# Kernel tuning notes

Measured on AMD Instinct MI355X. Metric: run time of the kernel, lower is better.

Reference implementation:

```python
import jax, jax.numpy as jnp
import numpy as np
import math

B, S, D_MODEL, D_K = 4, 4096, 1024, 256

def setup_inputs() -> dict:
    key = jax.random.key(0)
    ks = jax.random.split(key, 9)
    def xavier(k, shape):
        fan_out, fan_in = shape
        limit = math.sqrt(6.0 / (fan_in + fan_out))
        return jax.random.uniform(k, shape, jnp.float32, -limit, limit)
    return {
        "_q": jax.random.normal(ks[0], (B, S, D_MODEL), jnp.float32),
        "_k": jax.random.normal(ks[1], (B, S, D_MODEL), jnp.float32),
        "_v": jax.random.normal(ks[2], (B, S, D_MODEL), jnp.float32),
        "mask": jnp.ones((B, 1, S), dtype=bool),  # unused by the original forward
        "Wq": xavier(ks[3], (D_K, D_MODEL)),
        "bq": jnp.zeros((D_K,), jnp.float32),
        "Wk": xavier(ks[4], (D_K, D_MODEL)),
        "bk": jnp.zeros((D_K,), jnp.float32),
        "Wv": xavier(ks[5], (D_K, D_MODEL)),
        "bv": jnp.zeros((D_K,), jnp.float32),
    }

def reference(_q, _k, _v, mask, Wq, bq, Wk, bk, Wv, bv):
    # Linear projections: x @ W.T + b  (torch nn.Linear semantics)
    q = jnp.einsum('bsm,km->bsk', _q, Wq) + bq  # [B,S,d_k]
    k = jnp.einsum('bsm,km->bsk', _k, Wk) + bk
    v = jnp.einsum('bsm,km->bsk', _v, Wv) + bv
    scores = jnp.einsum('bqk,bsk->bqs', q, k) / math.sqrt(D_K)  # [B,S,S]
    atten = jax.nn.softmax(scores, axis=-1)
    out = jnp.einsum('bqs,bsk->bqk', atten, v)  # [B,S,d_k]
    return out
```

## Files before the change

### kernel.cpp

```cpp
#include <hip/hip_runtime.h>
#include <stdint.h>

#define DEV static __device__ __forceinline__

typedef __bf16 bf16x8 __attribute__((ext_vector_type(8)));
typedef float f32x4 __attribute__((ext_vector_type(4)));

typedef const __attribute__((address_space(1))) void* as1cp;
typedef __attribute__((address_space(3))) void* as3p;

DEV uint32_t f2bf1(float f) {
  uint32_t u = __builtin_bit_cast(uint32_t, f);
  u += 0x7fffu + ((u >> 16) & 1u);
  return u >> 16;
}
DEV uint32_t f2bf2(float lo, float hi) { return f2bf1(lo) | (f2bf1(hi) << 16); }
DEV float bf2f(uint32_t h) { return __builtin_bit_cast(float, h << 16); }

DEV void gll16(const void* g, void* l) {
  __builtin_amdgcn_global_load_lds((as1cp)g, (as3p)l, 16, 0, 0);
}

__global__ __launch_bounds__(256, 3) void proj_kernel(
    const float* __restrict__ xq, const float* __restrict__ xk, const float* __restrict__ xv,
    const float* __restrict__ wq, const float* __restrict__ wk, const float* __restrict__ wv,
    const float* __restrict__ bq, const float* __restrict__ bk, const float* __restrict__ bv,
    uint16_t* __restrict__ qo, uint16_t* __restrict__ ko, uint16_t* __restrict__ vo)
{
  const int z = blockIdx.z;
  const float* X  = (z == 0) ? xq : (z == 1) ? xk : xv;
  const float* W  = (z == 0) ? wq : (z == 1) ? wk : wv;
  const float* Bi = (z == 0) ? bq : (z == 1) ? bk : bv;

  const int tid = threadIdx.x;
  const int lane = tid & 63;
  const int w = tid >> 6;
  const int wm = w >> 1, wn = w & 1;
  const int l15 = lane & 15, g = lane >> 4;
  const int m0 = blockIdx.x * 128;
  const int n0 = blockIdx.y * 128;

  __shared__ uint16_t sA[128 * 64];
  __shared__ uint16_t sB[128 * 64];

  const int am = tid >> 1, ak = (tid & 1) * 32;
  const float* Ap = X + (size_t)(m0 + am) * 1024 + ak;
  const float* Wp = W + (size_t)(n0 + am) * 1024 + ak;

  f32x4 acc[4][4];
  #pragma unroll
  for (int i = 0; i < 4; ++i)
    #pragma unroll
    for (int j = 0; j < 4; ++j) { f32x4 zz = {0.f, 0.f, 0.f, 0.f}; acc[i][j] = zz; }

  float ar[32];
  #pragma unroll
  for (int i = 0; i < 8; ++i) { float4 t = ((const float4*)Ap)[i];
    ar[4*i+0]=t.x; ar[4*i+1]=t.y; ar[4*i+2]=t.z; ar[4*i+3]=t.w; }

  const uint32_t ph = (uint32_t)(am * 128 + ak * 2) ^ ((uint32_t)(am & 7) << 4);

  for (int kt = 0; kt < 16; ++kt) {
    if (kt) __syncthreads();
    #pragma unroll
    for (int c = 0; c < 4; ++c) {
      uint4 p;
      p.x = f2bf2(ar[8*c+0], ar[8*c+1]); p.y = f2bf2(ar[8*c+2], ar[8*c+3]);
      p.z = f2bf2(ar[8*c+4], ar[8*c+5]); p.w = f2bf2(ar[8*c+6], ar[8*c+7]);
      *(uint4*)((char*)sA + (ph ^ (16u * c))) = p;
    }
    {
      float wr[32];
      const float* Wk = Wp + kt * 64;
      #pragma unroll
      for (int i = 0; i < 8; ++i) { float4 t = ((const float4*)Wk)[i];
        wr[4*i+0]=t.x; wr[4*i+1]=t.y; wr[4*i+2]=t.z; wr[4*i+3]=t.w; }
      #pragma unroll
      for (int c = 0; c < 4; ++c) {
        uint4 p;
        p.x = f2bf2(wr[8*c+0], wr[8*c+1]); p.y = f2bf2(wr[8*c+2], wr[8*c+3]);
        p.z = f2bf2(wr[8*c+4], wr[8*c+5]); p.w = f2bf2(wr[8*c+6], wr[8*c+7]);
        *(uint4*)((char*)sB + (ph ^ (16u * c))) = p;
      }
    }
    __syncthreads();
    if (kt < 15) {
      const float* Ap2 = Ap + (kt + 1) * 64;
      #pragma unroll
      for (int i = 0; i < 8; ++i) { float4 t = ((const float4*)Ap2)[i];
        ar[4*i+0]=t.x; ar[4*i+1]=t.y; ar[4*i+2]=t.z; ar[4*i+3]=t.w; }
    }
    #pragma unroll
    for (int ks = 0; ks < 2; ++ks) {
      bf16x8 fa[4], fb[4];
      #pragma unroll
      for (int f = 0; f < 4; ++f) {
        uint32_t row = wm * 64 + 16 * f + l15;
        fa[f] = *(const bf16x8*)((char*)sA + row * 128 +
                 (((uint32_t)(ks * 64 + g * 16)) ^ ((row & 7) << 4)));
      }
      #pragma unroll
      for (int f = 0; f < 4; ++f) {
        uint32_t row = wn * 64 + 16 * f + l15;
        fb[f] = *(const bf16x8*)((char*)sB + row * 128 +
                 (((uint32_t)(ks * 64 + g * 16)) ^ ((row & 7) << 4)));
      }
      #pragma unroll
      for (int fm = 0; fm < 4; ++fm)
        #pragma unroll
        for (int fn = 0; fn < 4; ++fn)
          acc[fm][fn] = __builtin_amdgcn_mfma_f32_16x16x32_bf16(fa[fm], fb[fn], acc[fm][fn], 0, 0, 0);
    }
  }

  #pragma unroll
  for (int fn = 0; fn < 4; ++fn) {
    const int n = n0 + wn * 64 + 16 * fn + l15;
    const float bias = Bi[n];
    #pragma unroll
    for (int fm = 0; fm < 4; ++fm) {
      const int mg = m0 + wm * 64 + 16 * fm + 4 * g;
      if (z == 0) {
        #pragma unroll
        for (int r = 0; r < 4; ++r)
          qo[(size_t)(mg + r) * 256 + n] =
              (uint16_t)f2bf1((acc[fm][fn][r] + bias) * 0.09016844f);
      } else if (z == 1) {
        #pragma unroll
        for (int r = 0; r < 4; ++r)
          ko[(size_t)(mg + r) * 256 + n] = (uint16_t)f2bf1(acc[fm][fn][r] + bias);
      } else {
        uint2 pv;
        pv.x = f2bf2(acc[fm][fn][0] + bias, acc[fm][fn][1] + bias);
        pv.y = f2bf2(acc[fm][fn][2] + bias, acc[fm][fn][3] + bias);
        *(uint2*)(vo + (((size_t)(mg >> 12)) << 20) + (((size_t)n) << 12) + (mg & 4095)) = pv;
      }
    }
  }
}

__global__ __launch_bounds__(512) void attn_kernel(
    const uint16_t* __restrict__ qg, const uint16_t* __restrict__ kg,
    const uint16_t* __restrict__ vg, float* __restrict__ out)
{
  extern __shared__ char smem[];

  const int bid = blockIdx.x;
  const int xcd = bid & 7, slot = bid >> 3;
  const int batch = xcd >> 1;
  const int q0 = (((xcd & 1) << 5) + slot) * 64;

  const int tid = threadIdx.x;
  const int lane = tid & 63;
  const int w = tid >> 6;
  const int hv = w >> 2;
  const int wq = w & 3;
  const int l15 = lane & 15, g = lane >> 4;
  const size_t rowb = (size_t)batch * 4096;

  bf16x8 qf[8];
  {
    const uint16_t* qp = qg + (rowb + q0 + wq * 16 + l15) * 256;
    #pragma unroll
    for (int ks = 0; ks < 8; ++ks) qf[ks] = *(const bf16x8*)(qp + ks * 32 + g * 8);
  }

  f32x4 o[16];
  #pragma unroll
  for (int i = 0; i < 16; ++i) { f32x4 zz = {0.f, 0.f, 0.f, 0.f}; o[i] = zz; }
  float mrow[4], lrow[4];
  #pragma unroll
  for (int r = 0; r < 4; ++r) { mrow[r] = -1e30f; lrow[r] = 0.f; }

  const char* kgb = (const char*)(kg + rowb * 256);
  const char* vgb = (const char*)(vg + (size_t)batch * 256 * 4096);

  auto STAGE = [&](int h, int buf, int t) {
    const int kv0 = (2 * t + h) * 32;
    char* kd = smem + (size_t)(h * 2 + buf) * 16384;
    char* vd = smem + 65536 + (size_t)(h * 2 + buf) * 16384;
    #pragma unroll
    for (int r2 = 0; r2 < 2; ++r2) {
      uint32_t L = (uint32_t)(tid + r2 * 512) * 16;
      uint32_t U = L ^ (((L >> 9) & 7u) << 4);
      gll16(kgb + (size_t)(kv0 + (U >> 9)) * 512 + (U & 511), kd + L);
      uint32_t d = L >> 6;
      uint32_t kvo = (L >> 4) & 3u;
      gll16(vgb + (size_t)d * 8192 + (size_t)(kv0 + 8 * kvo) * 2, vd + L);
    }
  };

  STAGE(0, 0, 0); STAGE(1, 0, 0);
  char* Pw = smem + 131072 + (size_t)w * 1024;
  int buf = 0;

  for (int t = 0; t < 64; ++t) {
    __syncthreads();
    if (t + 1 < 64) { STAGE(0, buf ^ 1, t + 1); STAGE(1, buf ^ 1, t + 1); }

    const char* Kb = smem + (size_t)(hv * 2 + buf) * 16384;
    const char* Vb = smem + 65536 + (size_t)(hv * 2 + buf) * 16384;

    f32x4 s4[2];
    #pragma unroll
    for (int f = 0; f < 2; ++f) { f32x4 zz = {0.f, 0.f, 0.f, 0.f}; s4[f] = zz; }
    #pragma unroll
    for (int ks = 0; ks < 8; ++ks) {
      bf16x8 kf[2];
      #pragma unroll
      for (int f = 0; f < 2; ++f) {
        uint32_t row = 16 * f + l15;
        kf[f] = *(const bf16x8*)(Kb + row * 512 +
                 (((uint32_t)(ks * 64 + g * 16)) ^ ((l15 & 7) << 4)));
      }
      #pragma unroll
      for (int f = 0; f < 2; ++f)
        s4[f] = __builtin_amdgcn_mfma_f32_16x16x32_bf16(qf[ks], kf[f], s4[f], 0, 0, 0);
    }

    float mx[4];
    #pragma unroll
    for (int r = 0; r < 4; ++r) {
      float m2 = fmaxf(s4[0][r], s4[1][r]);
      m2 = fmaxf(m2, __shfl_xor(m2, 1, 64));
      m2 = fmaxf(m2, __shfl_xor(m2, 2, 64));
      m2 = fmaxf(m2, __shfl_xor(m2, 4, 64));
      m2 = fmaxf(m2, __shfl_xor(m2, 8, 64));
      mx[r] = m2;
    }
    int stable = (mx[0] <= mrow[0] + 8.f) && (mx[1] <= mrow[1] + 8.f) &&
                 (mx[2] <= mrow[2] + 8.f) && (mx[3] <= mrow[3] + 8.f);
    if (!__all(stable)) {
      float sc[4];
      #pragma unroll
      for (int r = 0; r < 4; ++r) {
        float mn = fmaxf(mrow[r], mx[r]);
        sc[r] = exp2f(mrow[r] - mn);
        mrow[r] = mn;
        lrow[r] *= sc[r];
      }
      #pragma unroll
      for (int j = 0; j < 16; ++j)
        #pragma unroll
        for (int r = 0; r < 4; ++r) o[j][r] *= sc[r];
    }
    float ps[2][4];
    #pragma unroll
    for (int r = 0; r < 4; ++r) {
      float sum = 0.f;
      #pragma unroll
      for (int f = 0; f < 2; ++f) { ps[f][r] = exp2f(s4[f][r] - mrow[r]); sum += ps[f][r]; }
      sum += __shfl_xor(sum, 1, 64);
      sum += __shfl_xor(sum, 2, 64);
      sum += __shfl_xor(sum, 4, 64);
      sum += __shfl_xor(sum, 8, 64);
      lrow[r] += sum;
    }

    #pragma unroll
    for (int f = 0; f < 2; ++f)
      #pragma unroll
      for (int r = 0; r < 4; ++r)
        *(uint16_t*)(Pw + (4 * g + r) * 64 +
            (((uint32_t)(32 * f + 2 * l15)) ^ ((uint32_t)g << 4))) = (uint16_t)f2bf1(ps[f][r]);

    bf16x8 pa = *(const bf16x8*)(Pw + l15 * 64 + 16 * (g ^ (l15 >> 2)));
    #pragma unroll
    for (int fd = 0; fd < 16; ++fd) {
      bf16x8 vbf = *(const bf16x8*)(Vb + fd * 1024 + l15 * 64 + g * 16);
      o[fd] = __builtin_amdgcn_mfma_f32_16x16x32_bf16(pa, vbf, o[fd], 0, 0, 0);
    }

    buf ^= 1;
  }

  float*    mlb = (float*)smem;
  uint32_t* ob  = (uint32_t*)(smem + 8192);
  __syncthreads();
  if (hv == 1) {
    #pragma unroll
    for (int r = 0; r < 4; ++r) {
      mlb[((0 * 4 + wq) * 64 + lane) * 4 + r] = mrow[r];
      mlb[((1 * 4 + wq) * 64 + lane) * 4 + r] = lrow[r];
    }
    #pragma unroll
    for (int fd = 0; fd < 16; ++fd)
      #pragma unroll
      for (int p = 0; p < 2; ++p)
        ob[(wq * 32 + fd * 2 + p) * 64 + lane] = f2bf2(o[fd][2 * p], o[fd][2 * p + 1]);
  }
  __syncthreads();
  if (hv == 0) {
    float a[4], b2[4], inv[4];
    #pragma unroll
    for (int r = 0; r < 4; ++r) {
      float mu = mlb[((0 * 4 + wq) * 64 + lane) * 4 + r];
      float lu = mlb[((1 * 4 + wq) * 64 + lane) * 4 + r];
      float mn = fmaxf(mrow[r], mu);
      a[r]  = exp2f(mrow[r] - mn);
      b2[r] = exp2f(mu - mn);
      inv[r] = 1.f / (lrow[r] * a[r] + lu * b2[r]);
    }
    float* op = out + (rowb + q0 + wq * 16) * 256;
    #pragma unroll
    for (int fd = 0; fd < 16; ++fd) {
      #pragma unroll
      for (int p = 0; p < 2; ++p) {
        uint32_t u = ob[(wq * 32 + fd * 2 + p) * 64 + lane];
        float vlo = bf2f(u & 0xffffu), vhi = bf2f(u >> 16);
        int r0 = 2 * p, r1 = 2 * p + 1;
        op[(4 * g + r0) * 256 + 16 * fd + l15] =
            (o[fd][r0] * a[r0] + vlo * b2[r0]) * inv[r0];
        op[(4 * g + r1) * 256 + 16 * fd + l15] =
            (o[fd][r1] * a[r1] + vhi * b2[r1]) * inv[r1];
      }
    }
  }
}

extern "C" void kernel_launch(void* const* d_in, const int* in_sizes, int n_in,
                              void* d_out, int out_size, void* d_ws, size_t ws_size,
                              hipStream_t stream) {
  const float* xq = (const float*)d_in[0];
  const float* xk = (const float*)d_in[1];
  const float* xv = (const float*)d_in[2];
  const float* wq = (const float*)d_in[4];
  const float* bq = (const float*)d_in[5];
  const float* wk = (const float*)d_in[6];
  const float* bk = (const float*)d_in[7];
  const float* wv = (const float*)d_in[8];
  const float* bv = (const float*)d_in[9];

  uint16_t* qws = (uint16_t*)d_ws;
  uint16_t* kws = qws + (size_t)4 * 4096 * 256;
  uint16_t* vws = kws + (size_t)4 * 4096 * 256;

  proj_kernel<<<dim3(128, 2, 3), 256, 0, stream>>>(
      xq, xk, xv, wq, wk, wv, bq, bk, bv, qws, kws, vws);

  (void)hipFuncSetAttribute((const void*)attn_kernel,
                            hipFuncAttributeMaxDynamicSharedMemorySize, 139264);
  attn_kernel<<<dim3(256), 512, 139264, stream>>>(qws, kws, vws, (float*)d_out);
}
```

Baseline: 446.6 us.

## Single-buffer attention K/V staging with precomputed offsets and smaller LDS

Replaces the double-buffered K/V LDS pipeline with one buffer that is refilled between two barriers at the end of each iteration. Global source offsets are precomputed once per thread, and V is laid out so each lane reads a contiguous 16-byte chunk. Dynamic shared memory drops from about 139KB to 73KB, and launch bounds now request higher occupancy. The cost is that global-to-LDS loads no longer overlap with MFMA compute; the grid is one block per CU, so the extra occupancy may not be usable. The tighter register budget from the launch bounds may also cause spills.

```diff
diff --git a/kernel.cpp b/kernel.cpp
--- a/kernel.cpp
+++ b/kernel.cpp
@@ -139,7 +139,7 @@
   }
 }
 
-__global__ __launch_bounds__(512) void attn_kernel(
+__global__ __launch_bounds__(512, 4) void attn_kernel(
     const uint16_t* __restrict__ qg, const uint16_t* __restrict__ kg,
     const uint16_t* __restrict__ vg, float* __restrict__ out)
 {
@@ -175,32 +175,34 @@
   const char* kgb = (const char*)(kg + rowb * 256);
   const char* vgb = (const char*)(vg + (size_t)batch * 256 * 4096);
 
-  auto STAGE = [&](int h, int buf, int t) {
-    const int kv0 = (2 * t + h) * 32;
-    char* kd = smem + (size_t)(h * 2 + buf) * 16384;
-    char* vd = smem + 65536 + (size_t)(h * 2 + buf) * 16384;
-    #pragma unroll
-    for (int r2 = 0; r2 < 2; ++r2) {
-      uint32_t L = (uint32_t)(tid + r2 * 512) * 16;
-      uint32_t U = L ^ (((L >> 9) & 7u) << 4);
-      gll16(kgb + (size_t)(kv0 + (U >> 9)) * 512 + (U & 511), kd + L);
-      uint32_t d = L >> 6;
-      uint32_t kvo = (L >> 4) & 3u;
-      gll16(vgb + (size_t)d * 8192 + (size_t)(kv0 + 8 * kvo) * 2, vd + L);
-    }
+  uint32_t ksrc[4], vsrc[4], sdst[4];
+  #pragma unroll
+  for (int r = 0; r < 4; ++r) {
+    uint32_t L = (uint32_t)(r * 512 + tid) * 16;
+    sdst[r] = L;
+    uint32_t row = (L >> 9) & 31, h = L >> 14;
+    ksrc[r] = (32 * h + row) * 512 + ((L & 511) ^ ((row & 7) << 4));
+    uint32_t fd = (L >> 10) & 15, g2 = (L >> 8) & 3, lv = (L >> 4) & 15;
+    vsrc[r] = (fd * 16 + lv) * 8192 + 64 * h + 16 * g2;
+  }
+
+  auto STAGE = [&](int t) {
+    const uint32_t kt = (uint32_t)t * 32768;
+    const uint32_t vt = (uint32_t)t * 128;
+    #pragma unroll
+    for (int r = 0; r < 4; ++r) gll16(kgb + kt + ksrc[r], smem + sdst[r]);
+    #pragma unroll
+    for (int r = 0; r < 4; ++r) gll16(vgb + vt + vsrc[r], smem + 32768 + sdst[r]);
   };
 
-  STAGE(0, 0, 0); STAGE(1, 0, 0);
-  char* Pw = smem + 131072 + (size_t)w * 1024;
-  int buf = 0;
+  STAGE(0);
+  __syncthreads();
+
+  const char* Kb = smem + hv * 16384;
+  const char* Vb = smem + 32768 + hv * 16384;
+  char* Pw = smem + 65536 + (size_t)w * 1024;
 
   for (int t = 0; t < 64; ++t) {
-    __syncthreads();
-    if (t + 1 < 64) { STAGE(0, buf ^ 1, t + 1); STAGE(1, buf ^ 1, t + 1); }
-
-    const char* Kb = smem + (size_t)(hv * 2 + buf) * 16384;
-    const char* Vb = smem + 65536 + (size_t)(hv * 2 + buf) * 16384;
-
     f32x4 s4[2];
     #pragma unroll
     for (int f = 0; f < 2; ++f) { f32x4 zz = {0.f, 0.f, 0.f, 0.f}; s4[f] = zz; }
@@ -267,16 +269,17 @@
     bf16x8 pa = *(const bf16x8*)(Pw + l15 * 64 + 16 * (g ^ (l15 >> 2)));
     #pragma unroll
     for (int fd = 0; fd < 16; ++fd) {
-      bf16x8 vbf = *(const bf16x8*)(Vb + fd * 1024 + l15 * 64 + g * 16);
+      bf16x8 vbf = *(const bf16x8*)(Vb + fd * 1024 + lane * 16);
       o[fd] = __builtin_amdgcn_mfma_f32_16x16x32_bf16(pa, vbf, o[fd], 0, 0, 0);
     }
 
-    buf ^= 1;
+    __syncthreads();
+    if (t + 1 < 64) STAGE(t + 1);
+    __syncthreads();
   }
 
   float*    mlb = (float*)smem;
   uint32_t* ob  = (uint32_t*)(smem + 8192);
-  __syncthreads();
   if (hv == 1) {
     #pragma unroll
     for (int r = 0; r < 4; ++r) {
@@ -339,6 +342,6 @@
       xq, xk, xv, wq, wk, wv, bq, bk, bv, qws, kws, vws);
 
   (void)hipFuncSetAttribute((const void*)attn_kernel,
-                            hipFuncAttributeMaxDynamicSharedMemorySize, 139264);
-  attn_kernel<<<dim3(256), 512, 139264, stream>>>(qws, kws, vws, (float*)d_out);
-}
+                            hipFuncAttributeMaxDynamicSharedMemorySize, 73728);
+  attn_kernel<<<dim3(256), 512, 73728, stream>>>(qws, kws, vws, (float*)d_out);
+}
```

Result: slower. 634.6 us (+42.1%).
